# Optimization experiments

Measured on AMD Instinct MI355X. Metric: run time of the kernel, lower is better.

## Reference

```python
import jax, jax.numpy as jnp
import numpy as np

B, N, F, H, L = 64, 8192, 64, 64, 2  # batch, max_nodes, feature_dim, hidden_dim, n_layers


def setup_inputs() -> dict:
    key = jax.random.key(0)
    k0, k1, k2 = jax.random.split(key, 3)
    s = 0.05
    return {
        "tree_features": jax.random.normal(k0, (B, N, F), dtype=jnp.float32),
        "W_emb": (jax.random.normal(k1, (H, F), dtype=jnp.float32) * s),
        "b_emb": jnp.zeros((H,), dtype=jnp.float32),
        # Wx[l, g] for g in (input, output, cell) gates; forget gate is dead when no children
        "Wx": (jax.random.normal(k2, (L, 3, H, H), dtype=jnp.float32) * s),
        "bW": jnp.zeros((L, 3, H), dtype=jnp.float32),
        # U(h_sum) with h_sum == 0 reduces to the U bias; U weights get zero grad, omitted
        "bU": jnp.zeros((L, 3, H), dtype=jnp.float32),
    }


def reference(tree_features, W_emb, b_emb, Wx, bW, bU):
    # node embedding: [B, N, F] @ [F, H]^T -> [B, N, H]
    h = jnp.einsum('bnf,hf->bnh', tree_features, W_emb) + b_emb
    n_layers = Wx.shape[0]
    for l in range(n_layers):
        # children_h is empty -> h_sum = 0, so U_*(h_sum) = bU (bias only)
        z = jnp.einsum('bni,goi->bngo', h, Wx[l]) + bW[l] + bU[l]  # [B, N, 3, H]
        i = jax.nn.sigmoid(z[:, :, 0])
        o = jax.nn.sigmoid(z[:, :, 1])
        c_tilde = jnp.tanh(z[:, :, 2])
        c = i * c_tilde  # no forget-gate terms: children_c is empty
        h = o * jnp.tanh(c)
    return jnp.mean(h, axis=1)  # [B, H]
```

## Files before the change

### kernel.cpp

```cpp
#include <hip/hip_runtime.h>
#include <hip/hip_bf16.h>


typedef __attribute__((ext_vector_type(4))) float f32x4;
typedef __attribute__((ext_vector_type(8))) short s16x8;
typedef __attribute__((ext_vector_type(2))) unsigned u32x2;
typedef __attribute__((ext_vector_type(4))) unsigned u32x4;
typedef _Float16 h2 __attribute__((ext_vector_type(2)));

__device__ __forceinline__ unsigned short f2h(float f) {
    _Float16 h = (_Float16)f;
    return __builtin_bit_cast(unsigned short, h);
}
__device__ __forceinline__ h2 pkrtz(float a, float b) {
    return __builtin_bit_cast(h2, __builtin_amdgcn_cvt_pkrtz(a, b));
}
__device__ __forceinline__ unsigned pk2(float a, float b) {
    return __builtin_bit_cast(unsigned, __builtin_amdgcn_cvt_pkrtz(a, b));
}
__device__ __forceinline__ h2 pfma(h2 a, h2 b, h2 c) {
    return __builtin_elementwise_fma(a, b, c);
}
#define H2C(v) h2{(_Float16)(v), (_Float16)(v)}

__device__ __forceinline__ h2 gate2(h2 z0, h2 z1, h2 z2) {
    const h2 C3 = H2C(-0.33333334f), C5 = H2C(0.13333334f), C7 = H2C(-0.05396825f);
    const h2 Q1 = H2C(0.25f), Q3 = H2C(-0.020833334f), Q5 = H2C(0.0020833334f);
    const h2 ONE = H2C(1.0f), HALF = H2C(0.5f);
    h2 s0 = z0 * z0, s1 = z1 * z1, s2 = z2 * z2;
    h2 sg0 = pfma(z0, pfma(pfma(Q5, s0, Q3), s0, Q1), HALF);
    h2 sg1 = pfma(z1, pfma(pfma(Q5, s1, Q3), s1, Q1), HALF);
    h2 t2  = z2 * pfma(pfma(pfma(C7, s2, C5), s2, C3), s2, ONE);
    h2 c   = sg0 * t2;
    h2 sc  = c * c;
    h2 th  = c * pfma(pfma(pfma(C7, sc, C5), sc, C3), sc, ONE);
    return sg1 * th;
}

__global__ void prep_weights(const float* __restrict__ W_emb,
                             const float* __restrict__ b_emb,
                             const float* __restrict__ Wx,
                             const float* __restrict__ bW,
                             const float* __restrict__ bU,
                             unsigned short* __restrict__ wfrag,
                             float* __restrict__ wbias) {
    int t = blockIdx.x * 256 + threadIdx.x;
    if (t < 448) {
        int mat = t >> 6, o = t & 63;
        wbias[t] = (mat == 0) ? b_emb[o] : (bW[(mat - 1) * 64 + o] + bU[(mat - 1) * 64 + o]);
    }
    if (t < 28672) {
        int j = t & 7, lane = (t >> 3) & 63, fid = t >> 9;
        int kk = fid & 1, wv = (fid >> 1) & 3, mat = fid >> 3;
        int o = wv * 16 + (lane & 15);
        int k = ((lane >> 4) << 3) + kk * 32 + j;
        float v = (mat == 0) ? W_emb[o * 64 + k] : Wx[(mat - 1) * 4096 + o * 64 + k];
        wfrag[t] = f2h(v);
    }
}

__global__ __launch_bounds__(256, 3) void tree_encoder_mfma(
        const float* __restrict__ tree,
        const unsigned short* __restrict__ wfrag,
        const float* __restrict__ wbias,
        float* __restrict__ out) {
    __shared__ unsigned short x16[4096];
    __shared__ unsigned short hA[4096], hB[4096];
    __shared__ float biasL[448];
    const int tid = threadIdx.x;
    const int w = tid >> 6, lane = tid & 63;
    const int lg = lane >> 4, lr = lane & 15;

    for (int i = tid; i < 448; i += 256) biasL[i] = wbias[i];

    s16x8 wA[14];
#pragma unroll
    for (int m = 0; m < 7; ++m)
#pragma unroll
        for (int kk = 0; kk < 2; ++kk)
            wA[m * 2 + kk] = *(const s16x8*)(wfrag + (((m * 4 + w) * 2 + kk) << 9) + lane * 8);
#pragma unroll
    for (int m = 0; m < 14; ++m) asm volatile("" : "+v"(wA[m]));

    int ro[4][2], wo[4];
#pragma unroll
    for (int nt = 0; nt < 4; ++nt) {
        const int n = nt * 16 + lr, sw = (n & 7) << 3;
        ro[nt][0] = (n << 6) + ((lg << 3) ^ sw);
        ro[nt][1] = (n << 6) + (((lg + 4) << 3) ^ sw);
        wo[nt] = (n << 6) + ((w * 16 + 4 * lg) ^ sw);
    }
    const int nc = tid >> 2;
    const int qc = tid & 3;
    const int co0 = (nc << 6) + (((2 * qc) ^ (nc & 7)) << 3);
    const int co1 = (nc << 6) + (((2 * qc + 1) ^ (nc & 7)) << 3);

    float nsum[4] = {0.f, 0.f, 0.f, 0.f};
    const int t0 = blockIdx.x * 4;

    f32x4 xp[4];
    {
        const float* src = tree + ((size_t)t0 << 12) + (tid << 4);
#pragma unroll
        for (int v = 0; v < 4; ++v) xp[v] = *(const f32x4*)(src + 4 * v);
    }

#pragma unroll 1
    for (int ti = 0; ti < 4; ++ti) {
        {
            u32x4 v0, v1;
            v0[0] = pk2(xp[0][0], xp[0][1]); v0[1] = pk2(xp[0][2], xp[0][3]);
            v0[2] = pk2(xp[1][0], xp[1][1]); v0[3] = pk2(xp[1][2], xp[1][3]);
            v1[0] = pk2(xp[2][0], xp[2][1]); v1[1] = pk2(xp[2][2], xp[2][3]);
            v1[2] = pk2(xp[3][0], xp[3][1]); v1[3] = pk2(xp[3][2], xp[3][3]);
            *(u32x4*)&x16[co0] = v0;
            *(u32x4*)&x16[co1] = v1;
        }
        if (ti < 3) {
            const float* src = tree + ((size_t)(t0 + ti + 1) << 12) + (tid << 4);
#pragma unroll
            for (int v = 0; v < 4; ++v) xp[v] = *(const f32x4*)(src + 4 * v);
        }
        __syncthreads();

        {
            const f32x4 be = *(const f32x4*)&biasL[w * 16 + 4 * lg];
            f32x4 acc[4];
#pragma unroll
            for (int nt = 0; nt < 4; ++nt) acc[nt] = be;
#pragma unroll
            for (int nt = 0; nt < 4; ++nt)
#pragma unroll
                for (int kk = 0; kk < 2; ++kk) {
                    s16x8 b = *(const s16x8*)&x16[ro[nt][kk]];
                    acc[nt] = __builtin_amdgcn_mfma_f32_16x16x32_f16(wA[kk], b, acc[nt], 0, 0, 0);
                }
#pragma unroll
            for (int nt = 0; nt < 4; ++nt) {
                u32x2 p;
                p[0] = pk2(acc[nt][0], acc[nt][1]);
                p[1] = pk2(acc[nt][2], acc[nt][3]);
                *(u32x2*)&hA[wo[nt]] = p;
            }
        }
        __syncthreads();

        {
            const f32x4 b0 = *(const f32x4*)&biasL[64 + w * 16 + 4 * lg];
            const f32x4 b1 = *(const f32x4*)&biasL[128 + w * 16 + 4 * lg];
            const f32x4 b2 = *(const f32x4*)&biasL[192 + w * 16 + 4 * lg];
#pragma unroll
            for (int nt = 0; nt < 4; ++nt) {
                f32x4 a0 = b0, a1 = b1, a2 = b2;
#pragma unroll
                for (int kk = 0; kk < 2; ++kk) {
                    s16x8 b = *(const s16x8*)&hA[ro[nt][kk]];
                    a0 = __builtin_amdgcn_mfma_f32_16x16x32_f16(wA[2 + kk], b, a0, 0, 0, 0);
                    a1 = __builtin_amdgcn_mfma_f32_16x16x32_f16(wA[4 + kk], b, a1, 0, 0, 0);
                    a2 = __builtin_amdgcn_mfma_f32_16x16x32_f16(wA[6 + kk], b, a2, 0, 0, 0);
                }
                h2 hlo = gate2(pkrtz(a0[0], a0[1]), pkrtz(a1[0], a1[1]), pkrtz(a2[0], a2[1]));
                h2 hhi = gate2(pkrtz(a0[2], a0[3]), pkrtz(a1[2], a1[3]), pkrtz(a2[2], a2[3]));
                u32x2 p;
                p[0] = __builtin_bit_cast(unsigned, hlo);
                p[1] = __builtin_bit_cast(unsigned, hhi);
                *(u32x2*)&hB[wo[nt]] = p;
            }
        }
        __syncthreads();

        {
            const f32x4 b0 = *(const f32x4*)&biasL[256 + w * 16 + 4 * lg];
            const f32x4 b1 = *(const f32x4*)&biasL[320 + w * 16 + 4 * lg];
            const f32x4 b2 = *(const f32x4*)&biasL[384 + w * 16 + 4 * lg];
#pragma unroll
            for (int nt = 0; nt < 4; ++nt) {
                f32x4 a0 = b0, a1 = b1, a2 = b2;
#pragma unroll
                for (int kk = 0; kk < 2; ++kk) {
                    s16x8 b = *(const s16x8*)&hB[ro[nt][kk]];
                    a0 = __builtin_amdgcn_mfma_f32_16x16x32_f16(wA[8 + kk], b, a0, 0, 0, 0);
                    a1 = __builtin_amdgcn_mfma_f32_16x16x32_f16(wA[10 + kk], b, a1, 0, 0, 0);
                    a2 = __builtin_amdgcn_mfma_f32_16x16x32_f16(wA[12 + kk], b, a2, 0, 0, 0);
                }
                h2 hlo = gate2(pkrtz(a0[0], a0[1]), pkrtz(a1[0], a1[1]), pkrtz(a2[0], a2[1]));
                h2 hhi = gate2(pkrtz(a0[2], a0[3]), pkrtz(a1[2], a1[3]), pkrtz(a2[2], a2[3]));
                nsum[0] += (float)hlo[0];
                nsum[1] += (float)hlo[1];
                nsum[2] += (float)hhi[0];
                nsum[3] += (float)hhi[1];
            }
        }
    }

#pragma unroll
    for (int r = 0; r < 4; ++r) {
        float s = nsum[r];
        s += __shfl_xor(s, 1);
        s += __shfl_xor(s, 2);
        s += __shfl_xor(s, 4);
        s += __shfl_xor(s, 8);
        if (lr == 0)
            atomicAdd(&out[(blockIdx.x >> 5) * 64 + w * 16 + 4 * lg + r], s * (1.0f / 8192.0f));
    }
}

extern "C" void kernel_launch(void* const* d_in, const int* in_sizes, int n_in,
                              void* d_out, int out_size, void* d_ws, size_t ws_size,
                              hipStream_t stream) {
    const float* tree  = (const float*)d_in[0];
    const float* W_emb = (const float*)d_in[1];
    const float* b_emb = (const float*)d_in[2];
    const float* Wx    = (const float*)d_in[3];
    const float* bW    = (const float*)d_in[4];
    const float* bU    = (const float*)d_in[5];
    float* outp = (float*)d_out;
    unsigned short* wfrag = (unsigned short*)d_ws;
    float* wbias = (float*)((char*)d_ws + 57344);

    (void)hipMemsetAsync(d_out, 0, (size_t)out_size * sizeof(float), stream);
    prep_weights<<<112, 256, 0, stream>>>(W_emb, b_emb, Wx, bW, bU, wfrag, wbias);
    tree_encoder_mfma<<<2048, 256, 0, stream>>>(tree, wfrag, wbias, outp);
}
```

Before: 59.23 us.

## Split block into two phase-shifted 256-thread halves to overlap pipeline stages

Blocks grow to 512 threads, made of two independent 256-thread sub-groups, each working on its own 4 tiles with private LDS buffers. The two halves run staggered stages (embedding, layer0, layer1, convert/prefetch), so one half's MFMA work overlaps the other's conversion and global loads within shared barriers. The intent is to hide load and convert latency and barrier stalls. The cost is double the LDS per block, a different occupancy bound (512,4), and barriers that now couple both halves.

```diff
diff --git a/kernel.cpp b/kernel.cpp
--- a/kernel.cpp
+++ b/kernel.cpp
@@ -59,19 +59,21 @@
     }
 }
 
-__global__ __launch_bounds__(256, 3) void tree_encoder_mfma(
+__global__ __launch_bounds__(512, 4) void tree_encoder_mfma(
         const float* __restrict__ tree,
         const unsigned short* __restrict__ wfrag,
         const float* __restrict__ wbias,
         float* __restrict__ out) {
-    __shared__ unsigned short x16[4096];
-    __shared__ unsigned short hA[4096], hB[4096];
+    __shared__ unsigned short xh[2][4096];
+    __shared__ unsigned short hAp[2][4096], hBp[2][4096];
     __shared__ float biasL[448];
     const int tid = threadIdx.x;
-    const int w = tid >> 6, lane = tid & 63;
+    const int s = tid >> 8;
+    const int w = (tid >> 6) & 3, lane = tid & 63;
     const int lg = lane >> 4, lr = lane & 15;
-
-    for (int i = tid; i < 448; i += 256) biasL[i] = wbias[i];
+    const int ltid = tid & 255;
+
+    for (int i = tid; i < 448; i += 512) biasL[i] = wbias[i];
 
     s16x8 wA[14];
 #pragma unroll
@@ -90,118 +92,130 @@
         ro[nt][1] = (n << 6) + (((lg + 4) << 3) ^ sw);
         wo[nt] = (n << 6) + ((w * 16 + 4 * lg) ^ sw);
     }
-    const int nc = tid >> 2;
-    const int qc = tid & 3;
+    const int nc = ltid >> 2;
+    const int qc = ltid & 3;
     const int co0 = (nc << 6) + (((2 * qc) ^ (nc & 7)) << 3);
     const int co1 = (nc << 6) + (((2 * qc + 1) ^ (nc & 7)) << 3);
 
+    unsigned short* xPl = xh[s];
+    unsigned short* hAPl = hAp[s];
+    unsigned short* hBPl = hBp[s];
+
     float nsum[4] = {0.f, 0.f, 0.f, 0.f};
-    const int t0 = blockIdx.x * 4;
+    const int tbase = blockIdx.x * 8 + s * 4;
 
     f32x4 xp[4];
-    {
-        const float* src = tree + ((size_t)t0 << 12) + (tid << 4);
+    auto PF = [&](int j) {
+        const float* src = tree + ((size_t)(tbase + j) << 12) + (ltid << 4);
 #pragma unroll
         for (int v = 0; v < 4; ++v) xp[v] = *(const f32x4*)(src + 4 * v);
-    }
-
+    };
+    auto CVT = [&]() {
+        u32x4 v0, v1;
+        v0[0] = pk2(xp[0][0], xp[0][1]); v0[1] = pk2(xp[0][2], xp[0][3]);
+        v0[2] = pk2(xp[1][0], xp[1][1]); v0[3] = pk2(xp[1][2], xp[1][3]);
+        v1[0] = pk2(xp[2][0], xp[2][1]); v1[1] = pk2(xp[2][2], xp[2][3]);
+        v1[2] = pk2(xp[3][0], xp[3][1]); v1[3] = pk2(xp[3][2], xp[3][3]);
+        *(u32x4*)&xPl[co0] = v0;
+        *(u32x4*)&xPl[co1] = v1;
+    };
+    auto EMB = [&]() {
+        const f32x4 be = *(const f32x4*)&biasL[w * 16 + 4 * lg];
+        f32x4 acc[4];
+#pragma unroll
+        for (int nt = 0; nt < 4; ++nt) acc[nt] = be;
+#pragma unroll
+        for (int nt = 0; nt < 4; ++nt)
+#pragma unroll
+            for (int kk = 0; kk < 2; ++kk) {
+                s16x8 b = *(const s16x8*)&xPl[ro[nt][kk]];
+                acc[nt] = __builtin_amdgcn_mfma_f32_16x16x32_f16(wA[kk], b, acc[nt], 0, 0, 0);
+            }
+#pragma unroll
+        for (int nt = 0; nt < 4; ++nt) {
+            u32x2 p;
+            p[0] = pk2(acc[nt][0], acc[nt][1]);
+            p[1] = pk2(acc[nt][2], acc[nt][3]);
+            *(u32x2*)&hAPl[wo[nt]] = p;
+        }
+    };
+    auto L0 = [&]() {
+        const f32x4 b0 = *(const f32x4*)&biasL[64 + w * 16 + 4 * lg];
+        const f32x4 b1 = *(const f32x4*)&biasL[128 + w * 16 + 4 * lg];
+        const f32x4 b2 = *(const f32x4*)&biasL[192 + w * 16 + 4 * lg];
+#pragma unroll
+        for (int nt = 0; nt < 4; ++nt) {
+            f32x4 a0 = b0, a1 = b1, a2 = b2;
+#pragma unroll
+            for (int kk = 0; kk < 2; ++kk) {
+                s16x8 b = *(const s16x8*)&hAPl[ro[nt][kk]];
+                a0 = __builtin_amdgcn_mfma_f32_16x16x32_f16(wA[2 + kk], b, a0, 0, 0, 0);
+                a1 = __builtin_amdgcn_mfma_f32_16x16x32_f16(wA[4 + kk], b, a1, 0, 0, 0);
+                a2 = __builtin_amdgcn_mfma_f32_16x16x32_f16(wA[6 + kk], b, a2, 0, 0, 0);
+            }
+            h2 hlo = gate2(pkrtz(a0[0], a0[1]), pkrtz(a1[0], a1[1]), pkrtz(a2[0], a2[1]));
+            h2 hhi = gate2(pkrtz(a0[2], a0[3]), pkrtz(a1[2], a1[3]), pkrtz(a2[2], a2[3]));
+            u32x2 p;
+            p[0] = __builtin_bit_cast(unsigned, hlo);
+            p[1] = __builtin_bit_cast(unsigned, hhi);
+            *(u32x2*)&hBPl[wo[nt]] = p;
+        }
+    };
+    auto L1 = [&]() {
+        const f32x4 b0 = *(const f32x4*)&biasL[256 + w * 16 + 4 * lg];
+        const f32x4 b1 = *(const f32x4*)&biasL[320 + w * 16 + 4 * lg];
+        const f32x4 b2 = *(const f32x4*)&biasL[384 + w * 16 + 4 * lg];
+#pragma unroll
+        for (int nt = 0; nt < 4; ++nt) {
+            f32x4 a0 = b0, a1 = b1, a2 = b2;
+#pragma unroll
+            for (int kk = 0; kk < 2; ++kk) {
+                s16x8 b = *(const s16x8*)&hBPl[ro[nt][kk]];
+                a0 = __builtin_amdgcn_mfma_f32_16x16x32_f16(wA[8 + kk], b, a0, 0, 0, 0);
+                a1 = __builtin_amdgcn_mfma_f32_16x16x32_f16(wA[10 + kk], b, a1, 0, 0, 0);
+                a2 = __builtin_amdgcn_mfma_f32_16x16x32_f16(wA[12 + kk], b, a2, 0, 0, 0);
+            }
+            h2 hlo = gate2(pkrtz(a0[0], a0[1]), pkrtz(a1[0], a1[1]), pkrtz(a2[0], a2[1]));
+            h2 hhi = gate2(pkrtz(a0[2], a0[3]), pkrtz(a1[2], a1[3]), pkrtz(a2[2], a2[3]));
+            nsum[0] += (float)hlo[0];
+            nsum[1] += (float)hlo[1];
+            nsum[2] += (float)hhi[0];
+            nsum[3] += (float)hhi[1];
+        }
+    };
+
+    PF(0);
+    if (s == 0) { CVT(); PF(1); }
+    __syncthreads();
+    if (s == 0) EMB(); else { CVT(); PF(1); }
+    __syncthreads();
 #pragma unroll 1
-    for (int ti = 0; ti < 4; ++ti) {
-        {
-            u32x4 v0, v1;
-            v0[0] = pk2(xp[0][0], xp[0][1]); v0[1] = pk2(xp[0][2], xp[0][3]);
-            v0[2] = pk2(xp[1][0], xp[1][1]); v0[3] = pk2(xp[1][2], xp[1][3]);
-            v1[0] = pk2(xp[2][0], xp[2][1]); v1[1] = pk2(xp[2][2], xp[2][3]);
-            v1[2] = pk2(xp[3][0], xp[3][1]); v1[3] = pk2(xp[3][2], xp[3][3]);
-            *(u32x4*)&x16[co0] = v0;
-            *(u32x4*)&x16[co1] = v1;
-        }
-        if (ti < 3) {
-            const float* src = tree + ((size_t)(t0 + ti + 1) << 12) + (tid << 4);
-#pragma unroll
-            for (int v = 0; v < 4; ++v) xp[v] = *(const f32x4*)(src + 4 * v);
-        }
-        __syncthreads();
-
-        {
-            const f32x4 be = *(const f32x4*)&biasL[w * 16 + 4 * lg];
-            f32x4 acc[4];
-#pragma unroll
-            for (int nt = 0; nt < 4; ++nt) acc[nt] = be;
-#pragma unroll
-            for (int nt = 0; nt < 4; ++nt)
-#pragma unroll
-                for (int kk = 0; kk < 2; ++kk) {
-                    s16x8 b = *(const s16x8*)&x16[ro[nt][kk]];
-                    acc[nt] = __builtin_amdgcn_mfma_f32_16x16x32_f16(wA[kk], b, acc[nt], 0, 0, 0);
-                }
-#pragma unroll
-            for (int nt = 0; nt < 4; ++nt) {
-                u32x2 p;
-                p[0] = pk2(acc[nt][0], acc[nt][1]);
-                p[1] = pk2(acc[nt][2], acc[nt][3]);
-                *(u32x2*)&hA[wo[nt]] = p;
-            }
-        }
-        __syncthreads();
-
-        {
-            const f32x4 b0 = *(const f32x4*)&biasL[64 + w * 16 + 4 * lg];
-            const f32x4 b1 = *(const f32x4*)&biasL[128 + w * 16 + 4 * lg];
-            const f32x4 b2 = *(const f32x4*)&biasL[192 + w * 16 + 4 * lg];
-#pragma unroll
-            for (int nt = 0; nt < 4; ++nt) {
-                f32x4 a0 = b0, a1 = b1, a2 = b2;
-#pragma unroll
-                for (int kk = 0; kk < 2; ++kk) {
-                    s16x8 b = *(const s16x8*)&hA[ro[nt][kk]];
-                    a0 = __builtin_amdgcn_mfma_f32_16x16x32_f16(wA[2 + kk], b, a0, 0, 0, 0);
-                    a1 = __builtin_amdgcn_mfma_f32_16x16x32_f16(wA[4 + kk], b, a1, 0, 0, 0);
-                    a2 = __builtin_amdgcn_mfma_f32_16x16x32_f16(wA[6 + kk], b, a2, 0, 0, 0);
-                }
-                h2 hlo = gate2(pkrtz(a0[0], a0[1]), pkrtz(a1[0], a1[1]), pkrtz(a2[0], a2[1]));
-                h2 hhi = gate2(pkrtz(a0[2], a0[3]), pkrtz(a1[2], a1[3]), pkrtz(a2[2], a2[3]));
-                u32x2 p;
-                p[0] = __builtin_bit_cast(unsigned, hlo);
-                p[1] = __builtin_bit_cast(unsigned, hhi);
-                *(u32x2*)&hB[wo[nt]] = p;
-            }
-        }
-        __syncthreads();
-
-        {
-            const f32x4 b0 = *(const f32x4*)&biasL[256 + w * 16 + 4 * lg];
-            const f32x4 b1 = *(const f32x4*)&biasL[320 + w * 16 + 4 * lg];
-            const f32x4 b2 = *(const f32x4*)&biasL[384 + w * 16 + 4 * lg];
-#pragma unroll
-            for (int nt = 0; nt < 4; ++nt) {
-                f32x4 a0 = b0, a1 = b1, a2 = b2;
-#pragma unroll
-                for (int kk = 0; kk < 2; ++kk) {
-                    s16x8 b = *(const s16x8*)&hB[ro[nt][kk]];
-                    a0 = __builtin_amdgcn_mfma_f32_16x16x32_f16(wA[8 + kk], b, a0, 0, 0, 0);
-                    a1 = __builtin_amdgcn_mfma_f32_16x16x32_f16(wA[10 + kk], b, a1, 0, 0, 0);
-                    a2 = __builtin_amdgcn_mfma_f32_16x16x32_f16(wA[12 + kk], b, a2, 0, 0, 0);
-                }
-                h2 hlo = gate2(pkrtz(a0[0], a0[1]), pkrtz(a1[0], a1[1]), pkrtz(a2[0], a2[1]));
-                h2 hhi = gate2(pkrtz(a0[2], a0[3]), pkrtz(a1[2], a1[3]), pkrtz(a2[2], a2[3]));
-                nsum[0] += (float)hlo[0];
-                nsum[1] += (float)hlo[1];
-                nsum[2] += (float)hhi[0];
-                nsum[3] += (float)hhi[1];
-            }
-        }
+    for (int k = 0; k < 4; ++k) {
+        if (s == 0) L0(); else EMB();
+        __syncthreads();
+        if (s == 0) L1(); else L0();
+        __syncthreads();
+        if (s == 0) {
+            if (k < 3) { CVT(); if (k < 2) PF(k + 2); }
+        } else L1();
+        __syncthreads();
+        if (s == 0) {
+            if (k < 3) EMB();
+        } else {
+            if (k < 3) { CVT(); if (k < 2) PF(k + 2); }
+        }
+        __syncthreads();
     }
 
 #pragma unroll
     for (int r = 0; r < 4; ++r) {
-        float s = nsum[r];
-        s += __shfl_xor(s, 1);
-        s += __shfl_xor(s, 2);
-        s += __shfl_xor(s, 4);
-        s += __shfl_xor(s, 8);
+        float v = nsum[r];
+        v += __shfl_xor(v, 1);
+        v += __shfl_xor(v, 2);
+        v += __shfl_xor(v, 4);
+        v += __shfl_xor(v, 8);
         if (lr == 0)
-            atomicAdd(&out[(blockIdx.x >> 5) * 64 + w * 16 + 4 * lg + r], s * (1.0f / 8192.0f));
+            atomicAdd(&out[(blockIdx.x >> 4) * 64 + w * 16 + 4 * lg + r], v * (1.0f / 8192.0f));
     }
 }
 
@@ -220,5 +234,5 @@
 
     (void)hipMemsetAsync(d_out, 0, (size_t)out_size * sizeof(float), stream);
     prep_weights<<<112, 256, 0, stream>>>(W_emb, b_emb, Wx, bW, bU, wfrag, wbias);
-    tree_encoder_mfma<<<2048, 256, 0, stream>>>(tree, wfrag, wbias, outp);
-}
+    tree_encoder_mfma<<<1024, 512, 0, stream>>>(tree, wfrag, wbias, outp);
+}
```

Result: slower. 73.90 us (+24.8%).
